# Kernel optimization log

Hardware: AMD Instinct MI355X
Metric: run time of the kernel (lower is better)

## Reference

```python
import jax, jax.numpy as jnp
import numpy as np

LABELS = (1, 2, 3)  # from init_kwargs
EPS = float(np.finfo(np.float32).eps)
SHAPE = (512, 512, 512)


def setup_inputs() -> dict:
    key = jax.random.key(0)
    k1, k2 = jax.random.split(key)
    # label maps with values in {0,1,2,3}, stored as float32 (equality-compared)
    vol1 = jax.random.randint(k1, SHAPE, 0, 4).astype(jnp.float32)
    vol2 = jax.random.randint(k2, SHAPE, 0, 4).astype(jnp.float32)
    return {"vol1": vol1, "vol2": vol2}


def reference(vol1, vol2):
    # Per-label Dice: dice_l = 2*|A_l & B_l| / (|A_l| + |B_l| + eps)
    dices = []
    for lab in LABELS:  # fixed tiny label set -> loop is fine
        labv = jnp.asarray(lab, dtype=vol1.dtype)
        m1 = vol1 == labv
        m2 = vol2 == labv
        top = 2.0 * jnp.sum(m1 & m2).astype(jnp.float32)
        bottom = jnp.sum(m1).astype(jnp.float32) + jnp.sum(m2).astype(jnp.float32)
        dices.append(top / (bottom + EPS))
    dicem = jnp.stack(dices)
    return 1.0 - jnp.mean(dicem)
```

## Files before the change

kernel.cpp:

```cpp
#include <hip/hip_runtime.h>


#define NCNT 9
#define UNROLL 4

typedef float v4f __attribute__((ext_vector_type(4)));

__global__ void dice_zero_ws(unsigned int* counters) {
    int i = threadIdx.x;
    if (i < NCNT) counters[i] = 0u;
}

__device__ __forceinline__ void count4(v4f x, v4f y, unsigned int* c) {
#pragma unroll
    for (int comp = 0; comp < 4; ++comp) {
        float xa = x[comp];
        float yb = y[comp];
        bool a1 = (xa == 1.0f), a2 = (xa == 2.0f), a3 = (xa == 3.0f);
        bool b1 = (yb == 1.0f), b2 = (yb == 2.0f), b3 = (yb == 3.0f);
        c[0] += a1; c[1] += a2; c[2] += a3;
        c[3] += b1; c[4] += b2; c[5] += b3;
        c[6] += a1 & b1; c[7] += a2 & b2; c[8] += a3 & b3;
    }
}

__global__ __launch_bounds__(256) void dice_count(const v4f* __restrict__ a,
                                                  const v4f* __restrict__ b,
                                                  unsigned int* __restrict__ counters,
                                                  int n4) {
    unsigned int c[NCNT];
#pragma unroll
    for (int k = 0; k < NCNT; ++k) c[k] = 0u;

    const int T = blockDim.x;
    const int per_block = (n4 / gridDim.x) & ~(T * UNROLL - 1);
    const int base = blockIdx.x * per_block;

    for (int j = 0; j < per_block; j += T * UNROLL) {
        const int i = base + j + (int)threadIdx.x;
        v4f x0 = __builtin_nontemporal_load(&a[i]);
        v4f x1 = __builtin_nontemporal_load(&a[i + T]);
        v4f x2 = __builtin_nontemporal_load(&a[i + 2 * T]);
        v4f x3 = __builtin_nontemporal_load(&a[i + 3 * T]);
        v4f y0 = __builtin_nontemporal_load(&b[i]);
        v4f y1 = __builtin_nontemporal_load(&b[i + T]);
        v4f y2 = __builtin_nontemporal_load(&b[i + 2 * T]);
        v4f y3 = __builtin_nontemporal_load(&b[i + 3 * T]);
        __builtin_amdgcn_sched_barrier(0);
        count4(x0, y0, c);
        count4(x1, y1, c);
        count4(x2, y2, c);
        count4(x3, y3, c);
    }

    const int done = per_block * gridDim.x;
    for (int i = done + blockIdx.x * T + (int)threadIdx.x; i < n4;
         i += gridDim.x * T) {
        count4(a[i], b[i], c);
    }

#pragma unroll
    for (int k = 0; k < NCNT; ++k) {
#pragma unroll
        for (int off = 32; off > 0; off >>= 1)
            c[k] += __shfl_down(c[k], off, 64);
    }

    __shared__ unsigned int s[4][NCNT];
    const int wave = threadIdx.x >> 6;
    const int lane = threadIdx.x & 63;
    if (lane == 0) {
#pragma unroll
        for (int k = 0; k < NCNT; ++k) s[wave][k] = c[k];
    }
    __syncthreads();
    if (threadIdx.x == 0) {
#pragma unroll
        for (int k = 0; k < NCNT; ++k) {
            unsigned int v = s[0][k] + s[1][k] + s[2][k] + s[3][k];
            atomicAdd(&counters[k], v);
        }
    }
}

__global__ void dice_finalize(const unsigned int* __restrict__ counters,
                              float* __restrict__ out) {
    const double eps = 1.1920928955078125e-07;
    double acc = 0.0;
#pragma unroll
    for (int l = 0; l < 3; ++l) {
        double c1 = (double)counters[l];
        double c2 = (double)counters[3 + l];
        double in = (double)counters[6 + l];
        acc += (2.0 * in) / (c1 + c2 + eps);
    }
    out[0] = (float)(1.0 - acc / 3.0);
}

extern "C" void kernel_launch(void* const* d_in, const int* in_sizes, int n_in,
                              void* d_out, int out_size, void* d_ws, size_t ws_size,
                              hipStream_t stream) {
    const float* v1 = (const float*)d_in[0];
    const float* v2 = (const float*)d_in[1];
    float* out = (float*)d_out;
    unsigned int* counters = (unsigned int*)d_ws;

    const int n = in_sizes[0];
    const int n4 = n >> 2;

    dice_zero_ws<<<1, 64, 0, stream>>>(counters);

    const int threads = 256;
    const int blocks = 2048;
    dice_count<<<blocks, threads, 0, stream>>>(
        (const v4f*)v1, (const v4f*)v2, counters, n4);

    dice_finalize<<<1, 1, 0, stream>>>(counters, out);
}
```

Baseline: 1.047 ms.

## Software-pipeline loads with register double buffering and raise occupancy hint

The count loop now prefetches the next two float4 pairs per input while counting the current pair, in place of issuing four pairs of loads and then counting them. The aim is to overlap memory latency with compare/count work inside each wave, and launch_bounds(256,8) asks for higher occupancy. Each block's chunk is now a multiple of 512 float4s instead of 1024, so the strided tail loop handles less leftover work. The risks are fewer loads in flight per wave and register pressure from the occupancy hint. The kernel hardcodes 256 threads per block, which matches the launch.

```diff
diff --git a/kernel.cpp b/kernel.cpp
--- a/kernel.cpp
+++ b/kernel.cpp
@@ -2,7 +2,6 @@
 
 
 #define NCNT 9
-#define UNROLL 4
 
 typedef float v4f __attribute__((ext_vector_type(4)));
 
@@ -24,39 +23,46 @@
     }
 }
 
-__global__ __launch_bounds__(256) void dice_count(const v4f* __restrict__ a,
-                                                  const v4f* __restrict__ b,
-                                                  unsigned int* __restrict__ counters,
-                                                  int n4) {
+__global__ __launch_bounds__(256, 8) void dice_count(const v4f* __restrict__ a,
+                                                     const v4f* __restrict__ b,
+                                                     unsigned int* __restrict__ counters,
+                                                     int n4) {
     unsigned int c[NCNT];
 #pragma unroll
     for (int k = 0; k < NCNT; ++k) c[k] = 0u;
 
-    const int T = blockDim.x;
-    const int per_block = (n4 / gridDim.x) & ~(T * UNROLL - 1);
+    const int T = 256;
+    const int STEP = 2 * T;
+    const int per_block = (n4 / gridDim.x) & ~(STEP - 1);
     const int base = blockIdx.x * per_block;
+    const int iters = per_block / STEP;
 
-    for (int j = 0; j < per_block; j += T * UNROLL) {
-        const int i = base + j + (int)threadIdx.x;
-        v4f x0 = __builtin_nontemporal_load(&a[i]);
-        v4f x1 = __builtin_nontemporal_load(&a[i + T]);
-        v4f x2 = __builtin_nontemporal_load(&a[i + 2 * T]);
-        v4f x3 = __builtin_nontemporal_load(&a[i + 3 * T]);
-        v4f y0 = __builtin_nontemporal_load(&b[i]);
-        v4f y1 = __builtin_nontemporal_load(&b[i + T]);
-        v4f y2 = __builtin_nontemporal_load(&b[i + 2 * T]);
-        v4f y3 = __builtin_nontemporal_load(&b[i + 3 * T]);
+    int i = base + (int)threadIdx.x;
+
+    v4f x0 = __builtin_nontemporal_load(&a[i]);
+    v4f x1 = __builtin_nontemporal_load(&a[i + T]);
+    v4f y0 = __builtin_nontemporal_load(&b[i]);
+    v4f y1 = __builtin_nontemporal_load(&b[i + T]);
+
+    for (int it = 1; it < iters; ++it) {
+        const int j = i + STEP;
+        v4f nx0 = __builtin_nontemporal_load(&a[j]);
+        v4f nx1 = __builtin_nontemporal_load(&a[j + T]);
+        v4f ny0 = __builtin_nontemporal_load(&b[j]);
+        v4f ny1 = __builtin_nontemporal_load(&b[j + T]);
         __builtin_amdgcn_sched_barrier(0);
         count4(x0, y0, c);
         count4(x1, y1, c);
-        count4(x2, y2, c);
-        count4(x3, y3, c);
+        x0 = nx0; x1 = nx1; y0 = ny0; y1 = ny1;
+        i = j;
     }
+    count4(x0, y0, c);
+    count4(x1, y1, c);
 
     const int done = per_block * gridDim.x;
-    for (int i = done + blockIdx.x * T + (int)threadIdx.x; i < n4;
-         i += gridDim.x * T) {
-        count4(a[i], b[i], c);
+    for (int r = done + blockIdx.x * T + (int)threadIdx.x; r < n4;
+         r += gridDim.x * T) {
+        count4(a[r], b[r], c);
     }
 
 #pragma unroll
```

New measurement: 1.062 ms. No clear change (+1.4%).
